# Kernel optimization log

Measured on AMD Instinct MI355X. Metric: run time of the kernel, lower is better.

## Reference

```python
import jax, jax.numpy as jnp
import numpy as np

LN_EPS = 1e-5

def _layernorm(x, g, b):
    mu = jnp.mean(x, axis=-1, keepdims=True)
    var = jnp.mean((x - mu) ** 2, axis=-1, keepdims=True)
    return (x - mu) * jax.lax.rsqrt(var + LN_EPS) * g + b

def _linear_init(k, fan_in, fan_out):
    s = 1.0 / np.sqrt(fan_in)
    kw, kb = jax.random.split(k)
    W = jax.random.uniform(kw, (fan_in, fan_out), jnp.float32, -s, s)
    b = jax.random.uniform(kb, (fan_out,), jnp.float32, -s, s)
    return W, b

def setup_inputs() -> dict:
    key = jax.random.key(0)
    ks = jax.random.split(key, 8)
    B, C, H, W = 4, 256, 64, 64
    Cout = 256
    N = H * W
    E = 16 * N
    x = jax.random.normal(ks[0], (B, C, H, W), jnp.float32)
    edge_index = jax.random.randint(ks[1], (2, E), 0, N)
    W1, b1 = _linear_init(ks[2], C, 1024)
    W2, b2 = _linear_init(ks[3], 1024, 512)
    W3, b3 = _linear_init(ks[4], 512, Cout)
    return {
        'x': x, 'edge_index': edge_index,
        'W1': W1, 'b1': b1, 'g1': jnp.ones(1024, jnp.float32), 'be1': jnp.zeros(1024, jnp.float32),
        'W2': W2, 'b2': b2, 'g2': jnp.ones(512, jnp.float32), 'be2': jnp.zeros(512, jnp.float32),
        'W3': W3, 'b3': b3, 'g_out': jnp.ones(Cout, jnp.float32), 'b_out': jnp.zeros(Cout, jnp.float32),
    }

def reference(x, edge_index, W1, b1, g1, be1, W2, b2, g2, be2, W3, b3, g_out, b_out):
    B, C, H, Wd = x.shape
    N = H * Wd
    # [B, N, C] node features (pixels as nodes)
    x_flat = x.reshape(B, C, N).transpose(0, 2, 1)
    # Dense adjacency from edge list (duplicates sum, same as sparse->to_dense).
    # Identical for every batch item, so build once and broadcast through einsum.
    A = jnp.zeros((N, N), x.dtype).at[edge_index[0], edge_index[1]].add(1.0)
    A = A + jnp.eye(N, dtype=x.dtype)  # self-loops
    deg = jnp.sum(A, axis=-1)
    d_inv_sqrt = jnp.where(deg > 0, jax.lax.rsqrt(deg), 0.0)
    A_norm = d_inv_sqrt[:, None] * A * d_inv_sqrt[None, :]
    # message passing: [N,N] @ [B,N,C] -> [B,N,C]
    h = jnp.einsum('mn,bnc->bmc', A_norm, x_flat)
    h = _layernorm(jax.nn.relu(h @ W1 + b1), g1, be1)
    h = _layernorm(jax.nn.relu(h @ W2 + b2), g2, be2)
    h = h @ W3 + b3
    h = _layernorm(h, g_out, b_out)
    return h.transpose(0, 2, 1).reshape(B, -1, H, Wd)
```

## Files before the change

### kernel.cpp

```cpp
#include <hip/hip_runtime.h>

typedef __attribute__((ext_vector_type(8))) short short8_t;
typedef __attribute__((ext_vector_type(4))) float f32x4;

#define AS1 __attribute__((address_space(1)))
#define AS3 __attribute__((address_space(3)))

static_assert(sizeof(short8_t) == 16, "short8_t must be 16B");

__device__ __forceinline__ short f2bf(float f) {
  union { float f; unsigned u; } v; v.f = f;
  unsigned r = (v.u + 0x7FFFu + ((v.u >> 16) & 1u)) >> 16;
  return (short)r;
}
__device__ __forceinline__ float bf2f(short s) {
  union { unsigned u; float f; } v; v.u = ((unsigned)(unsigned short)s) << 16;
  return v.f;
}

__global__ __launch_bounds__(256) void count_deg(const int* __restrict__ ei,
                                                 int* __restrict__ deg, int E) {
  int e = blockIdx.x * 256 + threadIdx.x;
  if (e < E) atomicAdd(&deg[ei[e]], 1);
}

__global__ __launch_bounds__(1024) void scan_deg(const int* __restrict__ deg,
                                                 int* __restrict__ rp,
                                                 float* __restrict__ dis) {
  __shared__ int part[1024];
  const int t = threadIdx.x;
  int4 v = ((const int4*)deg)[t];
  const int s = v.x + v.y + v.z + v.w;
  part[t] = s;
  __syncthreads();
  for (int off = 1; off < 1024; off <<= 1) {
    int mine = part[t];
    int add = (t >= off) ? part[t - off] : 0;
    __syncthreads();
    part[t] = mine + add;
    __syncthreads();
  }
  const int excl = part[t] - s;
  const int b4 = t * 4;
  rp[b4 + 0] = excl;
  rp[b4 + 1] = excl + v.x;
  rp[b4 + 2] = excl + v.x + v.y;
  rp[b4 + 3] = excl + v.x + v.y + v.z;
  if (t == 1023) rp[4096] = part[1023];
  dis[b4 + 0] = rsqrtf((float)(v.x + 1));
  dis[b4 + 1] = rsqrtf((float)(v.y + 1));
  dis[b4 + 2] = rsqrtf((float)(v.z + 1));
  dis[b4 + 3] = rsqrtf((float)(v.w + 1));
}

__global__ __launch_bounds__(256) void fill_csr(const int* __restrict__ ei,
                                                const int* __restrict__ rp,
                                                int* __restrict__ fill,
                                                int* __restrict__ cols, int E) {
  int e = blockIdx.x * 256 + threadIdx.x;
  if (e < E) {
    int r = ei[e];
    int c = ei[E + e];
    int p = atomicAdd(&fill[r], 1);
    cols[rp[r] + p] = c;
  }
}

__global__ __launch_bounds__(256) void xpose_scale(const float* __restrict__ x,
                                                   const float* __restrict__ dis,
                                                   float* __restrict__ xs) {
  __shared__ float tile[32][33];
  const int b = blockIdx.z;
  const int n0 = blockIdx.x * 32;
  const int c0 = blockIdx.y * 32;
  const int tx = threadIdx.x, ty = threadIdx.y;
  const float* xb = x + (long)b * 256 * 4096;
#pragma unroll
  for (int i = 0; i < 32; i += 8)
    tile[ty + i][tx] = xb[(long)(c0 + ty + i) * 4096 + n0 + tx];
  __syncthreads();
  float* xsb = xs + (long)b * 4096 * 256;
#pragma unroll
  for (int i = 0; i < 32; i += 8) {
    const int n = n0 + ty + i;
    xsb[(long)n * 256 + c0 + tx] = tile[tx][ty + i] * dis[n];
  }
}

__global__ __launch_bounds__(64) void gather_mp(const float* __restrict__ xs,
                                                const float* __restrict__ dis,
                                                const int* __restrict__ rp,
                                                const int* __restrict__ cols,
                                                short* __restrict__ h0) {
  const int bm = blockIdx.x;
  const int m = bm & 4095;
  const int t = threadIdx.x;
  const float4* xsb = (const float4*)(xs + ((long)(bm >> 12)) * 4096 * 256);
  float4 a = xsb[(long)m * 64 + t];
  const int s = rp[m], e = rp[m + 1];
  for (int j = s; j < e; ++j) {
    const int n = cols[j];
    float4 v = xsb[(long)n * 64 + t];
    a.x += v.x; a.y += v.y; a.z += v.z; a.w += v.w;
  }
  const float d = dis[m];
  short4 o;
  o.x = f2bf(a.x * d); o.y = f2bf(a.y * d); o.z = f2bf(a.z * d); o.w = f2bf(a.w * d);
  ((short4*)(h0 + (long)bm * 256))[t] = o;
}

__global__ __launch_bounds__(256) void wt_cast(const float* __restrict__ Wf,
                                               short* __restrict__ Wt, int K, int N) {
  __shared__ float tile[32][33];
  const int k0 = blockIdx.x * 32;
  const int n0 = blockIdx.y * 32;
  const int tx = threadIdx.x, ty = threadIdx.y;
#pragma unroll
  for (int i = 0; i < 32; i += 8)
    tile[ty + i][tx] = Wf[(long)(k0 + ty + i) * N + n0 + tx];
  __syncthreads();
#pragma unroll
  for (int i = 0; i < 32; i += 8)
    Wt[(long)(n0 + ty + i) * K + k0 + tx] = f2bf(tile[tx][ty + i]);
}

template <bool RELU>
__global__ __launch_bounds__(256, 2) void gemm_bf16(const short* __restrict__ A,
                                                    const short* __restrict__ Bt,
                                                    const float* __restrict__ bias,
                                                    short* __restrict__ out,
                                                    int M, int N, int K) {
  __shared__ __align__(16) short As[128 * 32];
  __shared__ __align__(16) short Bs[128 * 32];
  const int tid = threadIdx.x;
  const int lane = tid & 63;
  const int wave = tid >> 6;
  const int wm = wave >> 1;
  const int wn = wave & 1;
  const int m0 = blockIdx.x * 128;
  const int n0 = blockIdx.y * 128;

  f32x4 acc[4][4] = {};

  const int srow = wave * 32 + (lane >> 2);
  const int scol = (lane & 3) * 8;
  const short* ag = A + (long)(m0 + srow) * K + scol;
  const short* bg = Bt + (long)(n0 + srow) * K + scol;
  short* asl = &As[(wave * 32) * 32];
  short* bsl = &Bs[(wave * 32) * 32];

  const int fr = lane & 15;
  const int kc = (lane >> 4) * 8;

  for (int k0 = 0; k0 < K; k0 += 32) {
    __syncthreads();
    __builtin_amdgcn_global_load_lds((const AS1 void*)(ag + k0), (AS3 void*)asl, 16, 0, 0);
    __builtin_amdgcn_global_load_lds((const AS1 void*)(ag + k0 + 16 * K),
                                     (AS3 void*)(asl + 16 * 32), 16, 0, 0);
    __builtin_amdgcn_global_load_lds((const AS1 void*)(bg + k0), (AS3 void*)bsl, 16, 0, 0);
    __builtin_amdgcn_global_load_lds((const AS1 void*)(bg + k0 + 16 * K),
                                     (AS3 void*)(bsl + 16 * 32), 16, 0, 0);
    __syncthreads();

    short8_t af[4], bf[4];
#pragma unroll
    for (int i = 0; i < 4; ++i)
      af[i] = *(const short8_t*)&As[(wm * 64 + i * 16 + fr) * 32 + kc];
#pragma unroll
    for (int i = 0; i < 4; ++i)
      bf[i] = *(const short8_t*)&Bs[(wn * 64 + i * 16 + fr) * 32 + kc];
#pragma unroll
    for (int mi = 0; mi < 4; ++mi)
#pragma unroll
      for (int ni = 0; ni < 4; ++ni)
        acc[mi][ni] = __builtin_amdgcn_mfma_f32_16x16x32_bf16(af[mi], bf[ni],
                                                              acc[mi][ni], 0, 0, 0);
  }

  const int rq = (lane >> 4) * 4;
#pragma unroll
  for (int mi = 0; mi < 4; ++mi) {
#pragma unroll
    for (int ni = 0; ni < 4; ++ni) {
      const int col = n0 + wn * 64 + ni * 16 + fr;
      const float bv = bias[col];
#pragma unroll
      for (int r = 0; r < 4; ++r) {
        const int row = m0 + wm * 64 + mi * 16 + rq + r;
        float v = acc[mi][ni][r] + bv;
        if (RELU) v = fmaxf(v, 0.0f);
        out[(long)row * N + col] = f2bf(v);
      }
    }
  }
}

template <int L, bool OUTF32>
__global__ __launch_bounds__(256) void ln_rows(const short* __restrict__ in,
                                               const float* __restrict__ g,
                                               const float* __restrict__ be,
                                               void* __restrict__ outv) {
  const int lane = threadIdx.x & 63;
  const int w = threadIdx.x >> 6;
  const long row = (long)blockIdx.x * 4 + w;
  const short* p = in + row * L;
  constexpr int V = L / 256;
  float x[V * 4];
  float sum = 0.f, sq = 0.f;
#pragma unroll
  for (int i = 0; i < V; ++i) {
    short4 s = ((const short4*)p)[lane + i * 64];
    float a = bf2f(s.x), b = bf2f(s.y), c = bf2f(s.z), d = bf2f(s.w);
    x[i * 4 + 0] = a; x[i * 4 + 1] = b; x[i * 4 + 2] = c; x[i * 4 + 3] = d;
    sum += a + b + c + d;
    sq += a * a + b * b + c * c + d * d;
  }
#pragma unroll
  for (int off = 32; off > 0; off >>= 1) {
    sum += __shfl_xor(sum, off);
    sq += __shfl_xor(sq, off);
  }
  const float mu = sum * (1.0f / L);
  float var = sq * (1.0f / L) - mu * mu;
  var = fmaxf(var, 0.0f);
  const float inv = rsqrtf(var + 1e-5f);
#pragma unroll
  for (int i = 0; i < V; ++i) {
    float4 gv = ((const float4*)g)[lane + i * 64];
    float4 bv = ((const float4*)be)[lane + i * 64];
    float y0 = (x[i * 4 + 0] - mu) * inv * gv.x + bv.x;
    float y1 = (x[i * 4 + 1] - mu) * inv * gv.y + bv.y;
    float y2 = (x[i * 4 + 2] - mu) * inv * gv.z + bv.z;
    float y3 = (x[i * 4 + 3] - mu) * inv * gv.w + bv.w;
    if constexpr (OUTF32) {
      float4 o; o.x = y0; o.y = y1; o.z = y2; o.w = y3;
      ((float4*)((float*)outv + row * L))[lane + i * 64] = o;
    } else {
      short4 o; o.x = f2bf(y0); o.y = f2bf(y1); o.z = f2bf(y2); o.w = f2bf(y3);
      ((short4*)((short*)outv + row * L))[lane + i * 64] = o;
    }
  }
}

__global__ __launch_bounds__(256) void xpose_out(const float* __restrict__ y,
                                                 float* __restrict__ out) {
  __shared__ float tile[32][33];
  const int b = blockIdx.z;
  const int n0 = blockIdx.x * 32;
  const int c0 = blockIdx.y * 32;
  const int tx = threadIdx.x, ty = threadIdx.y;
#pragma unroll
  for (int i = 0; i < 32; i += 8)
    tile[ty + i][tx] = y[(long)b * 4096 * 256 + (long)(n0 + ty + i) * 256 + c0 + tx];
  __syncthreads();
#pragma unroll
  for (int i = 0; i < 32; i += 8)
    out[(long)b * 256 * 4096 + (long)(c0 + ty + i) * 4096 + n0 + tx] = tile[tx][ty + i];
}

extern "C" void kernel_launch(void* const* d_in, const int* in_sizes, int n_in,
                              void* d_out, int out_size, void* d_ws, size_t ws_size,
                              hipStream_t stream) {
  (void)n_in; (void)out_size; (void)ws_size;
  const float* x   = (const float*)d_in[0];
  const int*   ei  = (const int*)d_in[1];
  const float* W1  = (const float*)d_in[2];
  const float* b1  = (const float*)d_in[3];
  const float* g1  = (const float*)d_in[4];
  const float* be1 = (const float*)d_in[5];
  const float* W2  = (const float*)d_in[6];
  const float* b2  = (const float*)d_in[7];
  const float* g2  = (const float*)d_in[8];
  const float* be2 = (const float*)d_in[9];
  const float* W3  = (const float*)d_in[10];
  const float* b3  = (const float*)d_in[11];
  const float* go  = (const float*)d_in[12];
  const float* bo  = (const float*)d_in[13];
  float* out = (float*)d_out;
  const int E = in_sizes[1] / 2;

  char* w = (char*)d_ws;
  int*   deg  = (int*)(w + 0);
  int*   fil  = (int*)(w + (16 << 10));
  int*   rp   = (int*)(w + (32 << 10));
  float* dis  = (float*)(w + (64 << 10));
  int*   cols = (int*)(w + (80 << 10));
  short* w1t  = (short*)(w + (512 << 10));
  short* w2t  = (short*)(w + (1 << 20));
  short* w3t  = (short*)(w + (2 << 20));
  char* RA = w + (4ull << 20);
  char* RB = w + (36ull << 20);
  char* RC = w + (52ull << 20);
  float* xs = (float*)RA;
  short* h0 = (short*)RB;
  short* t1 = (short*)RC;
  short* h1 = (short*)RA;
  short* t2 = (short*)RB;
  short* h2 = (short*)RC;
  short* t3 = (short*)RB;
  float* y3 = (float*)RA;

  hipMemsetAsync(d_ws, 0, 32 << 10, stream);
  count_deg<<<(E + 255) / 256, 256, 0, stream>>>(ei, deg, E);
  scan_deg<<<1, 1024, 0, stream>>>(deg, rp, dis);
  fill_csr<<<(E + 255) / 256, 256, 0, stream>>>(ei, rp, fil, cols, E);
  wt_cast<<<dim3(8, 32), dim3(32, 8), 0, stream>>>(W1, w1t, 256, 1024);
  wt_cast<<<dim3(32, 16), dim3(32, 8), 0, stream>>>(W2, w2t, 1024, 512);
  wt_cast<<<dim3(16, 8), dim3(32, 8), 0, stream>>>(W3, w3t, 512, 256);
  xpose_scale<<<dim3(128, 8, 4), dim3(32, 8), 0, stream>>>(x, dis, xs);
  gather_mp<<<16384, 64, 0, stream>>>(xs, dis, rp, cols, h0);
  gemm_bf16<true><<<dim3(128, 8), 256, 0, stream>>>(h0, w1t, b1, t1, 16384, 1024, 256);
  ln_rows<1024, false><<<4096, 256, 0, stream>>>(t1, g1, be1, (void*)h1);
  gemm_bf16<true><<<dim3(128, 4), 256, 0, stream>>>(h1, w2t, b2, t2, 16384, 512, 1024);
  ln_rows<512, false><<<4096, 256, 0, stream>>>(t2, g2, be2, (void*)h2);
  gemm_bf16<false><<<dim3(128, 2), 256, 0, stream>>>(h2, w3t, b3, t3, 16384, 256, 512);
  ln_rows<256, true><<<4096, 256, 0, stream>>>(t3, go, bo, (void*)y3);
  xpose_out<<<dim3(128, 8, 4), dim3(32, 8), 0, stream>>>(y3, out);
}
```

Measured before the change: 156.7 us.

## Fold layernorms into GEMM epilogues, merge prep kernels, bf16 batched gather

Each layernorm is folded algebraically into the next GEMM. The gamma scale goes into the weights, and column sums cs/ct together with per-row sum and sum-of-squares stats (accumulated atomically in the previous GEMM's epilogue) apply the mean and rstd. This removes the standalone ln_rows passes. CSR fill, the input transpose and the weight casts are merged into one prep launch. The gather now stores xs in bf16, interleaved across the batch, so one block serves all four batches of a node. The GEMM gets double-buffered LDS loads, and the final layernorm is fused with the output transpose. The risks are extra atomics and precision loss from computing variance as E[x^2]-mu^2 on unnormalized activations.

```diff
diff --git a/kernel.cpp b/kernel.cpp
--- a/kernel.cpp
+++ b/kernel.cpp
@@ -53,92 +53,118 @@
   dis[b4 + 3] = rsqrtf((float)(v.w + 1));
 }
 
-__global__ __launch_bounds__(256) void fill_csr(const int* __restrict__ ei,
-                                                const int* __restrict__ rp,
-                                                int* __restrict__ fill,
-                                                int* __restrict__ cols, int E) {
-  int e = blockIdx.x * 256 + threadIdx.x;
-  if (e < E) {
-    int r = ei[e];
-    int c = ei[E + e];
-    int p = atomicAdd(&fill[r], 1);
-    cols[rp[r] + p] = c;
-  }
-}
-
-__global__ __launch_bounds__(256) void xpose_scale(const float* __restrict__ x,
-                                                   const float* __restrict__ dis,
-                                                   float* __restrict__ xs) {
+__global__ __launch_bounds__(256) void prep(
+    const int* __restrict__ ei, const int* __restrict__ rp, int* __restrict__ fil,
+    int* __restrict__ cols, int E,
+    const float* __restrict__ x, const float* __restrict__ dis, short* __restrict__ xs,
+    const float* __restrict__ W1, const float* __restrict__ W2, const float* __restrict__ W3,
+    const float* __restrict__ g1, const float* __restrict__ be1,
+    const float* __restrict__ g2, const float* __restrict__ be2,
+    short* __restrict__ w1t, short* __restrict__ w2t, short* __restrict__ w3t,
+    float* __restrict__ cs2, float* __restrict__ ct2,
+    float* __restrict__ cs3, float* __restrict__ ct3) {
   __shared__ float tile[32][33];
-  const int b = blockIdx.z;
-  const int n0 = blockIdx.x * 32;
-  const int c0 = blockIdx.y * 32;
   const int tx = threadIdx.x, ty = threadIdx.y;
-  const float* xb = x + (long)b * 256 * 4096;
+  const int bid = blockIdx.x;
+  if (bid < 256) {
+    const int e = bid * 256 + ty * 32 + tx;
+    if (e < E) {
+      const int r = ei[e], c = ei[E + e];
+      const int p = atomicAdd(&fil[r], 1);
+      cols[rp[r] + p] = c;
+    }
+    return;
+  }
+  if (bid < 256 + 4096) {
+    const int id = bid - 256;
+    const int b = id >> 10;
+    const int n0 = ((id & 1023) >> 3) * 32;
+    const int c0 = (id & 7) * 32;
+    const float* xb = x + (long)b * (256 * 4096);
+#pragma unroll
+    for (int i = 0; i < 32; i += 8)
+      tile[ty + i][tx] = xb[(long)(c0 + ty + i) * 4096 + n0 + tx];
+    __syncthreads();
+#pragma unroll
+    for (int i = 0; i < 32; i += 8) {
+      const int n = n0 + ty + i;
+      xs[(long)n * 1024 + b * 256 + c0 + tx] = f2bf(tile[tx][ty + i] * dis[n]);
+    }
+    return;
+  }
+  int id = bid - 4352;
+  const float *Wf, *g = nullptr, *be = nullptr;
+  float *cs = nullptr, *ctp = nullptr;
+  short* Wt;
+  int K, N, k0, n0;
+  if (id < 256)      { Wf = W1; Wt = w1t; K = 256;  N = 1024; k0 = (id & 7) * 32;  n0 = (id >> 3) * 32; }
+  else if (id < 768) { id -= 256; Wf = W2; Wt = w2t; K = 1024; N = 512; k0 = (id & 31) * 32; n0 = (id >> 5) * 32;
+                       g = g1; be = be1; cs = cs2; ctp = ct2; }
+  else               { id -= 768; Wf = W3; Wt = w3t; K = 512;  N = 256; k0 = (id & 15) * 32; n0 = (id >> 4) * 32;
+                       g = g2; be = be2; cs = cs3; ctp = ct3; }
+  float csp = 0.f, ctv = 0.f;
+#pragma unroll
+  for (int i = 0; i < 32; i += 8) {
+    const int k = k0 + ty + i;
+    const float wv = Wf[(long)k * N + n0 + tx];
+    const float gk = g ? g[k] : 1.0f;
+    tile[ty + i][tx] = gk * wv;
+    csp += gk * wv;
+    if (be) ctv += be[k] * wv;
+  }
+  __syncthreads();
 #pragma unroll
   for (int i = 0; i < 32; i += 8)
-    tile[ty + i][tx] = xb[(long)(c0 + ty + i) * 4096 + n0 + tx];
-  __syncthreads();
-  float* xsb = xs + (long)b * 4096 * 256;
-#pragma unroll
-  for (int i = 0; i < 32; i += 8) {
-    const int n = n0 + ty + i;
-    xsb[(long)n * 256 + c0 + tx] = tile[tx][ty + i] * dis[n];
-  }
-}
-
-__global__ __launch_bounds__(64) void gather_mp(const float* __restrict__ xs,
-                                                const float* __restrict__ dis,
-                                                const int* __restrict__ rp,
-                                                const int* __restrict__ cols,
-                                                short* __restrict__ h0) {
-  const int bm = blockIdx.x;
-  const int m = bm & 4095;
+    Wt[(long)(n0 + ty + i) * K + k0 + tx] = f2bf(tile[tx][ty + i]);
+  if (cs) {
+    atomicAdd(&cs[n0 + tx], csp);
+    atomicAdd(&ctp[n0 + tx], ctv);
+  }
+}
+
+__global__ __launch_bounds__(256) void gather_mp(const short* __restrict__ xs,
+                                                 const float* __restrict__ dis,
+                                                 const int* __restrict__ rp,
+                                                 const int* __restrict__ cols,
+                                                 short* __restrict__ h0) {
+  __shared__ int sc[256];
+  const int m = blockIdx.x;
   const int t = threadIdx.x;
-  const float4* xsb = (const float4*)(xs + ((long)(bm >> 12)) * 4096 * 256);
-  float4 a = xsb[(long)m * 64 + t];
+  short4 v0 = ((const short4*)(xs + (long)m * 1024))[t];
+  float a0 = bf2f(v0.x), a1 = bf2f(v0.y), a2 = bf2f(v0.z), a3 = bf2f(v0.w);
   const int s = rp[m], e = rp[m + 1];
-  for (int j = s; j < e; ++j) {
-    const int n = cols[j];
-    float4 v = xsb[(long)n * 64 + t];
-    a.x += v.x; a.y += v.y; a.z += v.z; a.w += v.w;
+  for (int base = s; base < e; base += 256) {
+    const int cnt = min(256, e - base);
+    __syncthreads();
+    if (t < cnt) sc[t] = cols[base + t];
+    __syncthreads();
+    for (int j = 0; j < cnt; ++j) {
+      const int n = sc[j];
+      short4 v = ((const short4*)(xs + (long)n * 1024))[t];
+      a0 += bf2f(v.x); a1 += bf2f(v.y); a2 += bf2f(v.z); a3 += bf2f(v.w);
+    }
   }
   const float d = dis[m];
   short4 o;
-  o.x = f2bf(a.x * d); o.y = f2bf(a.y * d); o.z = f2bf(a.z * d); o.w = f2bf(a.w * d);
-  ((short4*)(h0 + (long)bm * 256))[t] = o;
-}
-
-__global__ __launch_bounds__(256) void wt_cast(const float* __restrict__ Wf,
-                                               short* __restrict__ Wt, int K, int N) {
-  __shared__ float tile[32][33];
-  const int k0 = blockIdx.x * 32;
-  const int n0 = blockIdx.y * 32;
-  const int tx = threadIdx.x, ty = threadIdx.y;
-#pragma unroll
-  for (int i = 0; i < 32; i += 8)
-    tile[ty + i][tx] = Wf[(long)(k0 + ty + i) * N + n0 + tx];
-  __syncthreads();
-#pragma unroll
-  for (int i = 0; i < 32; i += 8)
-    Wt[(long)(n0 + ty + i) * K + k0 + tx] = f2bf(tile[tx][ty + i]);
-}
-
-template <bool RELU>
-__global__ __launch_bounds__(256, 2) void gemm_bf16(const short* __restrict__ A,
-                                                    const short* __restrict__ Bt,
-                                                    const float* __restrict__ bias,
-                                                    short* __restrict__ out,
-                                                    int M, int N, int K) {
-  __shared__ __align__(16) short As[128 * 32];
-  __shared__ __align__(16) short Bs[128 * 32];
+  o.x = f2bf(a0 * d); o.y = f2bf(a1 * d); o.z = f2bf(a2 * d); o.w = f2bf(a3 * d);
+  const int b = t >> 6, c4 = t & 63;
+  ((short4*)(h0 + (((long)b << 12) + m) * 256))[c4] = o;
+}
+
+template <bool LNIN, bool RELU>
+__global__ __launch_bounds__(256, 2) void gemm_ln(
+    const short* __restrict__ A, const short* __restrict__ Bt,
+    const float* __restrict__ bias, const float* __restrict__ cs,
+    const float* __restrict__ ct, const float* __restrict__ statsIn,
+    float* __restrict__ statsOut, short* __restrict__ out,
+    int M, int N, int K) {
+  __shared__ __align__(16) short As[2][128 * 32];
+  __shared__ __align__(16) short Bs[2][128 * 32];
   const int tid = threadIdx.x;
   const int lane = tid & 63;
   const int wave = tid >> 6;
-  const int wm = wave >> 1;
-  const int wn = wave & 1;
-  const int m0 = blockIdx.x * 128;
-  const int n0 = blockIdx.y * 128;
+  const int wm = wave >> 1, wn = wave & 1;
+  const int m0 = blockIdx.x * 128, n0 = blockIdx.y * 128;
 
   f32x4 acc[4][4] = {};
 
@@ -146,116 +172,127 @@
   const int scol = (lane & 3) * 8;
   const short* ag = A + (long)(m0 + srow) * K + scol;
   const short* bg = Bt + (long)(n0 + srow) * K + scol;
-  short* asl = &As[(wave * 32) * 32];
-  short* bsl = &Bs[(wave * 32) * 32];
-
+  const int ldst = (wave * 32) * 32;
   const int fr = lane & 15;
   const int kc = (lane >> 4) * 8;
-
-  for (int k0 = 0; k0 < K; k0 += 32) {
-    __syncthreads();
-    __builtin_amdgcn_global_load_lds((const AS1 void*)(ag + k0), (AS3 void*)asl, 16, 0, 0);
-    __builtin_amdgcn_global_load_lds((const AS1 void*)(ag + k0 + 16 * K),
-                                     (AS3 void*)(asl + 16 * 32), 16, 0, 0);
-    __builtin_amdgcn_global_load_lds((const AS1 void*)(bg + k0), (AS3 void*)bsl, 16, 0, 0);
-    __builtin_amdgcn_global_load_lds((const AS1 void*)(bg + k0 + 16 * K),
-                                     (AS3 void*)(bsl + 16 * 32), 16, 0, 0);
-    __syncthreads();
-
+  const int NT = K >> 5;
+
+#define STAGE(T, BUF)                                                                        \
+  do {                                                                                       \
+    const short* a_ = ag + (T) * 32;                                                         \
+    const short* b_ = bg + (T) * 32;                                                         \
+    __builtin_amdgcn_global_load_lds((const AS1 void*)a_, (AS3 void*)(&As[BUF][ldst]), 16, 0, 0); \
+    __builtin_amdgcn_global_load_lds((const AS1 void*)(a_ + 16 * K), (AS3 void*)(&As[BUF][ldst + 512]), 16, 0, 0); \
+    __builtin_amdgcn_global_load_lds((const AS1 void*)b_, (AS3 void*)(&Bs[BUF][ldst]), 16, 0, 0); \
+    __builtin_amdgcn_global_load_lds((const AS1 void*)(b_ + 16 * K), (AS3 void*)(&Bs[BUF][ldst + 512]), 16, 0, 0); \
+  } while (0)
+
+  STAGE(0, 0);
+  __syncthreads();
+  int cur = 0;
+  for (int t = 0; t < NT; ++t) {
+    if (t + 1 < NT) STAGE(t + 1, cur ^ 1);
     short8_t af[4], bf[4];
 #pragma unroll
     for (int i = 0; i < 4; ++i)
-      af[i] = *(const short8_t*)&As[(wm * 64 + i * 16 + fr) * 32 + kc];
+      af[i] = *(const short8_t*)&As[cur][(wm * 64 + i * 16 + fr) * 32 + kc];
 #pragma unroll
     for (int i = 0; i < 4; ++i)
-      bf[i] = *(const short8_t*)&Bs[(wn * 64 + i * 16 + fr) * 32 + kc];
+      bf[i] = *(const short8_t*)&Bs[cur][(wn * 64 + i * 16 + fr) * 32 + kc];
 #pragma unroll
     for (int mi = 0; mi < 4; ++mi)
 #pragma unroll
       for (int ni = 0; ni < 4; ++ni)
         acc[mi][ni] = __builtin_amdgcn_mfma_f32_16x16x32_bf16(af[mi], bf[ni],
                                                               acc[mi][ni], 0, 0, 0);
-  }
+    __syncthreads();
+    cur ^= 1;
+  }
+#undef STAGE
 
   const int rq = (lane >> 4) * 4;
+  const float invK = 1.0f / (float)K;
+  float bv[4], csv[4], ctv[4];
+#pragma unroll
+  for (int ni = 0; ni < 4; ++ni) {
+    const int col = n0 + wn * 64 + ni * 16 + fr;
+    bv[ni] = bias[col];
+    if (LNIN) { csv[ni] = cs[col]; ctv[ni] = ct[col]; }
+  }
 #pragma unroll
   for (int mi = 0; mi < 4; ++mi) {
+    float r1[4], rmu[4];
+    if (LNIN) {
+#pragma unroll
+      for (int r = 0; r < 4; ++r) {
+        const int row = m0 + wm * 64 + mi * 16 + rq + r;
+        const float s = statsIn[row * 2];
+        const float q = statsIn[row * 2 + 1];
+        const float mu = s * invK;
+        const float var = fmaxf(q * invK - mu * mu, 0.0f);
+        const float rr = rsqrtf(var + 1e-5f);
+        r1[r] = rr; rmu[r] = rr * mu;
+      }
+    }
+    float sv[4] = {0, 0, 0, 0}, qv[4] = {0, 0, 0, 0};
 #pragma unroll
     for (int ni = 0; ni < 4; ++ni) {
       const int col = n0 + wn * 64 + ni * 16 + fr;
-      const float bv = bias[col];
 #pragma unroll
       for (int r = 0; r < 4; ++r) {
         const int row = m0 + wm * 64 + mi * 16 + rq + r;
-        float v = acc[mi][ni][r] + bv;
+        float v = acc[mi][ni][r];
+        if (LNIN) v = r1[r] * v - rmu[r] * csv[ni] + ctv[ni] + bv[ni];
+        else      v = v + bv[ni];
         if (RELU) v = fmaxf(v, 0.0f);
         out[(long)row * N + col] = f2bf(v);
+        sv[r] += v; qv[r] += v * v;
       }
     }
-  }
-}
-
-template <int L, bool OUTF32>
-__global__ __launch_bounds__(256) void ln_rows(const short* __restrict__ in,
-                                               const float* __restrict__ g,
-                                               const float* __restrict__ be,
-                                               void* __restrict__ outv) {
-  const int lane = threadIdx.x & 63;
-  const int w = threadIdx.x >> 6;
-  const long row = (long)blockIdx.x * 4 + w;
-  const short* p = in + row * L;
-  constexpr int V = L / 256;
-  float x[V * 4];
-  float sum = 0.f, sq = 0.f;
-#pragma unroll
-  for (int i = 0; i < V; ++i) {
-    short4 s = ((const short4*)p)[lane + i * 64];
-    float a = bf2f(s.x), b = bf2f(s.y), c = bf2f(s.z), d = bf2f(s.w);
-    x[i * 4 + 0] = a; x[i * 4 + 1] = b; x[i * 4 + 2] = c; x[i * 4 + 3] = d;
-    sum += a + b + c + d;
-    sq += a * a + b * b + c * c + d * d;
-  }
-#pragma unroll
-  for (int off = 32; off > 0; off >>= 1) {
-    sum += __shfl_xor(sum, off);
-    sq += __shfl_xor(sq, off);
-  }
-  const float mu = sum * (1.0f / L);
-  float var = sq * (1.0f / L) - mu * mu;
-  var = fmaxf(var, 0.0f);
+#pragma unroll
+    for (int r = 0; r < 4; ++r) {
+      float s = sv[r], q = qv[r];
+#pragma unroll
+      for (int off = 1; off < 16; off <<= 1) {
+        s += __shfl_xor(s, off);
+        q += __shfl_xor(q, off);
+      }
+      if (fr == 0) {
+        const int row = m0 + wm * 64 + mi * 16 + rq + r;
+        atomicAdd(&statsOut[row * 2], s);
+        atomicAdd(&statsOut[row * 2 + 1], q);
+      }
+    }
+  }
+}
+
+__global__ __launch_bounds__(256) void ln_tr_out(const short* __restrict__ t3,
+                                                 const float* __restrict__ stats,
+                                                 const float* __restrict__ g,
+                                                 const float* __restrict__ be,
+                                                 float* __restrict__ out) {
+  __shared__ short tile[64][66];
+  const int tx = threadIdx.x;
+  const int ty = threadIdx.y;
+  const int n0 = blockIdx.x * 64;
+  const int c0 = blockIdx.y * 64;
+  const int b = blockIdx.z;
+  const long rbase = ((long)b << 12) + n0;
+#pragma unroll
+  for (int i = ty; i < 64; i += 4)
+    tile[i][tx] = t3[(rbase + i) * 256 + c0 + tx];
+  const float s = stats[(rbase + tx) * 2];
+  const float q = stats[(rbase + tx) * 2 + 1];
+  const float mu = s * (1.0f / 256.0f);
+  const float var = fmaxf(q * (1.0f / 256.0f) - mu * mu, 0.0f);
   const float inv = rsqrtf(var + 1e-5f);
-#pragma unroll
-  for (int i = 0; i < V; ++i) {
-    float4 gv = ((const float4*)g)[lane + i * 64];
-    float4 bv = ((const float4*)be)[lane + i * 64];
-    float y0 = (x[i * 4 + 0] - mu) * inv * gv.x + bv.x;
-    float y1 = (x[i * 4 + 1] - mu) * inv * gv.y + bv.y;
-    float y2 = (x[i * 4 + 2] - mu) * inv * gv.z + bv.z;
-    float y3 = (x[i * 4 + 3] - mu) * inv * gv.w + bv.w;
-    if constexpr (OUTF32) {
-      float4 o; o.x = y0; o.y = y1; o.z = y2; o.w = y3;
-      ((float4*)((float*)outv + row * L))[lane + i * 64] = o;
-    } else {
-      short4 o; o.x = f2bf(y0); o.y = f2bf(y1); o.z = f2bf(y2); o.w = f2bf(y3);
-      ((short4*)((short*)outv + row * L))[lane + i * 64] = o;
-    }
-  }
-}
-
-__global__ __launch_bounds__(256) void xpose_out(const float* __restrict__ y,
-                                                 float* __restrict__ out) {
-  __shared__ float tile[32][33];
-  const int b = blockIdx.z;
-  const int n0 = blockIdx.x * 32;
-  const int c0 = blockIdx.y * 32;
-  const int tx = threadIdx.x, ty = threadIdx.y;
-#pragma unroll
-  for (int i = 0; i < 32; i += 8)
-    tile[ty + i][tx] = y[(long)b * 4096 * 256 + (long)(n0 + ty + i) * 256 + c0 + tx];
   __syncthreads();
-#pragma unroll
-  for (int i = 0; i < 32; i += 8)
-    out[(long)b * 256 * 4096 + (long)(c0 + ty + i) * 4096 + n0 + tx] = tile[tx][ty + i];
+  float* ob = out + ((long)b << 20) + n0 + tx;
+#pragma unroll
+  for (int i = ty; i < 64; i += 4) {
+    const int c = c0 + i;
+    ob[(long)c * 4096] = (bf2f(tile[tx][i]) - mu) * inv * g[c] + be[c];
+  }
 }
 
 extern "C" void kernel_launch(void* const* d_in, const int* in_sizes, int n_in,
@@ -280,40 +317,39 @@
   const int E = in_sizes[1] / 2;
 
   char* w = (char*)d_ws;
-  int*   deg  = (int*)(w + 0);
-  int*   fil  = (int*)(w + (16 << 10));
-  int*   rp   = (int*)(w + (32 << 10));
-  float* dis  = (float*)(w + (64 << 10));
-  int*   cols = (int*)(w + (80 << 10));
-  short* w1t  = (short*)(w + (512 << 10));
-  short* w2t  = (short*)(w + (1 << 20));
-  short* w3t  = (short*)(w + (2 << 20));
-  char* RA = w + (4ull << 20);
-  char* RB = w + (36ull << 20);
-  char* RC = w + (52ull << 20);
-  float* xs = (float*)RA;
-  short* h0 = (short*)RB;
-  short* t1 = (short*)RC;
-  short* h1 = (short*)RA;
-  short* t2 = (short*)RB;
-  short* h2 = (short*)RC;
-  short* t3 = (short*)RB;
-  float* y3 = (float*)RA;
-
-  hipMemsetAsync(d_ws, 0, 32 << 10, stream);
-  count_deg<<<(E + 255) / 256, 256, 0, stream>>>(ei, deg, E);
+  int*   deg    = (int*)(w + 0);
+  int*   fil    = (int*)(w + (16 << 10));
+  float* stats1 = (float*)(w + (32 << 10));
+  float* stats2 = (float*)(w + (160 << 10));
+  float* stats3 = (float*)(w + (288 << 10));
+  float* cs2    = (float*)(w + (416 << 10));
+  float* ct2    = (float*)(w + (418 << 10));
+  float* cs3    = (float*)(w + (420 << 10));
+  float* ct3    = (float*)(w + (421 << 10));
+  int*   rp   = (int*)(w + (424 << 10));
+  float* dis  = (float*)(w + (444 << 10));
+  int*   cols = (int*)(w + (460 << 10));
+  short* w1t  = (short*)(w + (720 << 10));
+  short* w2t  = (short*)(w + (1240 << 10));
+  short* w3t  = (short*)(w + (2264 << 10));
+  short* xs   = (short*)(w + (3ull << 20));
+  short* h0   = (short*)(w + (11ull << 20));
+  short* t1   = (short*)(w + (19ull << 20));
+  short* t2   = (short*)(w + (51ull << 20));
+  short* t3   = (short*)(w + (67ull << 20));
+
+  hipMemsetAsync(d_ws, 0, 422 << 10, stream);
+  count_deg<<<256, 256, 0, stream>>>(ei, deg, E);
   scan_deg<<<1, 1024, 0, stream>>>(deg, rp, dis);
-  fill_csr<<<(E + 255) / 256, 256, 0, stream>>>(ei, rp, fil, cols, E);
-  wt_cast<<<dim3(8, 32), dim3(32, 8), 0, stream>>>(W1, w1t, 256, 1024);
-  wt_cast<<<dim3(32, 16), dim3(32, 8), 0, stream>>>(W2, w2t, 1024, 512);
-  wt_cast<<<dim3(16, 8), dim3(32, 8), 0, stream>>>(W3, w3t, 512, 256);
-  xpose_scale<<<dim3(128, 8, 4), dim3(32, 8), 0, stream>>>(x, dis, xs);
-  gather_mp<<<16384, 64, 0, stream>>>(xs, dis, rp, cols, h0);
-  gemm_bf16<true><<<dim3(128, 8), 256, 0, stream>>>(h0, w1t, b1, t1, 16384, 1024, 256);
-  ln_rows<1024, false><<<4096, 256, 0, stream>>>(t1, g1, be1, (void*)h1);
-  gemm_bf16<true><<<dim3(128, 4), 256, 0, stream>>>(h1, w2t, b2, t2, 16384, 512, 1024);
-  ln_rows<512, false><<<4096, 256, 0, stream>>>(t2, g2, be2, (void*)h2);
-  gemm_bf16<false><<<dim3(128, 2), 256, 0, stream>>>(h2, w3t, b3, t3, 16384, 256, 512);
-  ln_rows<256, true><<<4096, 256, 0, stream>>>(t3, go, bo, (void*)y3);
-  xpose_out<<<dim3(128, 8, 4), dim3(32, 8), 0, stream>>>(y3, out);
-}
+  prep<<<5248, dim3(32, 8), 0, stream>>>(ei, rp, fil, cols, E, x, dis, xs,
+                                         W1, W2, W3, g1, be1, g2, be2,
+                                         w1t, w2t, w3t, cs2, ct2, cs3, ct3);
+  gather_mp<<<4096, 256, 0, stream>>>(xs, dis, rp, cols, h0);
+  gemm_ln<false, true><<<dim3(128, 8), 256, 0, stream>>>(
+      h0, w1t, b1, nullptr, nullptr, nullptr, stats1, t1, 16384, 1024, 256);
+  gemm_ln<true, true><<<dim3(128, 4), 256, 0, stream>>>(
+      t1, w2t, b2, cs2, ct2, stats1, stats2, t2, 16384, 512, 1024);
+  gemm_ln<true, false><<<dim3(128, 2), 256, 0, stream>>>(
+      t2, w3t, b3, cs3, ct3, stats2, stats3, t3, 16384, 256, 512);
+  ln_tr_out<<<dim3(64, 4, 4), dim3(64, 4), 0, stream>>>(t3, stats3, go, bo, out);
+}
```

After: 147.7 us. -5.7%, faster.
